# Optimization experiments

Hardware: AMD Instinct MI355X
Metric: run time of the kernel (lower is better)

Reference implementation:

```python
import jax, jax.numpy as jnp
import numpy as np

HIDDEN = 4096
N_HEAD = 16
HEAD_DIM = HIDDEN // N_HEAD          # 256
ROTARY_DIM = HEAD_DIM // 2           # 128 (partial rotary, GPT-J config)
ROPE_BASE = 10000.0
B, S = 4, 1024


def _apply_rope(x, position_ids):
    # x: [B, S, H, D]; rotate first ROTARY_DIM dims, NeoX/rotate-half style.
    rot, pas = x[..., :ROTARY_DIM], x[..., ROTARY_DIM:]
    inv_freq = 1.0 / (ROPE_BASE ** (jnp.arange(0, ROTARY_DIM, 2, dtype=jnp.float32) / ROTARY_DIM))
    ang = position_ids.astype(jnp.float32)[..., None] * inv_freq      # [B, S, R/2]
    cos = jnp.cos(ang)[:, :, None, :]                                  # [B, S, 1, R/2]
    sin = jnp.sin(ang)[:, :, None, :]
    x1, x2 = rot[..., : ROTARY_DIM // 2], rot[..., ROTARY_DIM // 2:]
    rot_out = jnp.concatenate([x1 * cos - x2 * sin, x2 * cos + x1 * sin], axis=-1)
    return jnp.concatenate([rot_out, pas], axis=-1)


def setup_inputs() -> dict:
    key = jax.random.key(0)
    k1, k2, k3 = jax.random.split(key, 3)
    hidden_states = jax.random.normal(k1, (B, S, HIDDEN), dtype=jnp.float32)
    w_qkv = jax.random.normal(k2, (HIDDEN, 3 * HIDDEN), dtype=jnp.float32) * (HIDDEN ** -0.5)
    w_out = jax.random.normal(k3, (HIDDEN, HIDDEN), dtype=jnp.float32) * (HIDDEN ** -0.5)
    position_ids = jnp.broadcast_to(jnp.arange(S, dtype=jnp.int32)[None, :], (B, S))
    return {"position_ids": position_ids, "hidden_states": hidden_states,
            "w_qkv": w_qkv, "w_out": w_out}


def reference(position_ids, hidden_states, w_qkv, w_out):
    qkv = hidden_states @ w_qkv                       # [B, S, 3H]
    q, k, v = jnp.split(qkv, 3, axis=-1)
    q = q.reshape(B, S, N_HEAD, HEAD_DIM)
    k = k.reshape(B, S, N_HEAD, HEAD_DIM)
    v = v.reshape(B, S, N_HEAD, HEAD_DIM)
    q = _apply_rope(q, position_ids)
    k = _apply_rope(k, position_ids)
    scale = HEAD_DIM ** -0.5
    scores = jnp.einsum('bqhd,bkhd->bhqk', q, k) * scale   # [B, H, S, S]
    causal = jnp.tril(jnp.ones((S, S), dtype=bool))
    scores = jnp.where(causal[None, None], scores, jnp.finfo(scores.dtype).min)
    probs = jax.nn.softmax(scores, axis=-1)
    attn = jnp.einsum('bhqk,bkhd->bqhd', probs, v).reshape(B, S, HIDDEN)
    return attn @ w_out
```

## Files before the change

kernel.cpp:

```cpp
#include <hip/hip_runtime.h>
#include <cstdint>

#define HID  4096
#define NHD  16
#define HDIM 256
#define SEQ  1024
#define BB   4
#define N3   12288
#define TOK  4096

typedef unsigned short u16;
typedef __bf16 bf16x8 __attribute__((ext_vector_type(8)));
typedef float  f32x4  __attribute__((ext_vector_type(4)));
typedef float  f32x16 __attribute__((ext_vector_type(16)));

__device__ __forceinline__ u16 f2b(float f) {
    unsigned u = __builtin_bit_cast(unsigned, f);
    u += 0x7fffu + ((u >> 16) & 1u);
    return (u16)(u >> 16);
}
__device__ __forceinline__ float b2f(u16 v) {
    unsigned u = ((unsigned)v) << 16;
    return __builtin_bit_cast(float, u);
}
__device__ __forceinline__ unsigned cvt_pk_bf16(float lo, float hi) {
    unsigned r;
    asm("v_cvt_pk_bf16_f32 %0, %1, %2" : "=v"(r) : "v"(lo), "v"(hi));
    return r;
}

typedef __attribute__((address_space(3))) unsigned       lds_u32;
typedef const __attribute__((address_space(1))) unsigned glb_u32;
__device__ __forceinline__ void async16(const void* g, void* l) {
    __builtin_amdgcn_global_load_lds((glb_u32*)g, (lds_u32*)l, 16, 0, 0);
}

__global__ __launch_bounds__(256) void cast_bf16(const float4* __restrict__ in,
                                                 uint4* __restrict__ out, int n8) {
    int i = blockIdx.x * 256 + threadIdx.x;
    if (i >= n8) return;
    float4 a = in[2 * i], b = in[2 * i + 1];
    union { u16 h[8]; uint4 v; } o;
    o.h[0] = f2b(a.x); o.h[1] = f2b(a.y); o.h[2] = f2b(a.z); o.h[3] = f2b(a.w);
    o.h[4] = f2b(b.x); o.h[5] = f2b(b.y); o.h[6] = f2b(b.z); o.h[7] = f2b(b.w);
    out[i] = o.v;
}

__global__ __launch_bounds__(256) void tcast(const float* __restrict__ in,
                                             u16* __restrict__ out, int R, int C) {
    __shared__ u16 sT[64 * 80];
    const int c0 = blockIdx.x * 64, r0 = blockIdx.y * 64;
    const int t = threadIdx.x;
    const int rr = t >> 4, cc = (t & 15) * 4;
    for (int rnd = 0; rnd < 4; rnd++) {
        int r = rnd * 16 + rr;
        float4 v = *(const float4*)(in + (size_t)(r0 + r) * C + c0 + cc);
        sT[(cc + 0) * 80 + r] = f2b(v.x);
        sT[(cc + 1) * 80 + r] = f2b(v.y);
        sT[(cc + 2) * 80 + r] = f2b(v.z);
        sT[(cc + 3) * 80 + r] = f2b(v.w);
    }
    __syncthreads();
    const int orow = t >> 2, oc = (t & 3) * 16;
    u16* dst = out + (size_t)(c0 + orow) * R + r0 + oc;
    *(uint4*)dst       = *(uint4*)&sT[orow * 80 + oc];
    *(uint4*)(dst + 8) = *(uint4*)&sT[orow * 80 + oc + 8];
}

template <bool OUT_BF16>
__global__ __launch_bounds__(512, 2) void gemm256(const u16* __restrict__ A,
                                                  const u16* __restrict__ Bt,
                                                  void* __restrict__ Cout,
                                                  int M, int N, int K) {
    __shared__ alignas(16) u16 lds[65536];
    const int t = threadIdx.x;
    const int lane = t & 63, w = t >> 6;
    const int wm = w >> 2, wn = w & 3;
    const int fm = lane & 15, g = lane >> 4;

    const int nwg = (int)gridDim.x;
    const int cpx = nwg >> 3;
    const int swz = (((int)blockIdx.x) & 7) * cpx + (((int)blockIdx.x) >> 3);
    const int gm = M >> 8;
    const int mblk = swz % gm, nblk = swz / gm;
    const int m0 = mblk << 8, n0 = nblk << 8;

    const int srow = t >> 2;
    const int schk = ((t & 3) ^ (srow & 3) ^ ((srow >> 2) & 2)) * 8;
    const u16* gA = A  + (size_t)(m0 + srow) * K + schk;
    const u16* gB = Bt + (size_t)(n0 + srow) * K + schk;
    const size_t hstep = (size_t)128 * K;
    const int ldst = t * 8;

    const int cxor = (g ^ (fm & 3) ^ ((fm >> 2) & 2)) * 8;
    const int aoff = (wm * 128 + fm) * 32 + cxor;
    const int boff = 16384 + (wn * 64 + fm) * 32 + cxor;

    f32x4 acc[8][4];
#pragma unroll
    for (int i = 0; i < 8; i++)
#pragma unroll
        for (int j = 0; j < 4; j++) acc[i][j] = f32x4{0.f, 0.f, 0.f, 0.f};

    const int nk = K >> 6;

#define STG_A(BO, KT, KS) do { \
    const u16* s_ = gA + (size_t)(KT) * 64 + (KS) * 32; \
    async16(s_,         &lds[(BO) + (KS) * 8192 + ldst]); \
    async16(s_ + hstep, &lds[(BO) + (KS) * 8192 + 4096 + ldst]); } while (0)
#define STG_B(BO, KT, KS) do { \
    const u16* s_ = gB + (size_t)(KT) * 64 + (KS) * 32; \
    async16(s_,         &lds[(BO) + 16384 + (KS) * 8192 + ldst]); \
    async16(s_ + hstep, &lds[(BO) + 16384 + (KS) * 8192 + 4096 + ldst]); } while (0)

    bf16x8 a0[4], a1[4], bfr[4];

#define LD_A0(BO, KS) { _Pragma("unroll") for (int m_ = 0; m_ < 4; m_++) \
    a0[m_] = *(const bf16x8*)&lds[(BO) + (KS) * 8192 + aoff + m_ * 512]; }
#define LD_A1(BO, KS) { _Pragma("unroll") for (int m_ = 0; m_ < 4; m_++) \
    a1[m_] = *(const bf16x8*)&lds[(BO) + (KS) * 8192 + 2048 + aoff + m_ * 512]; }
#define LD_B(BO, KS) { _Pragma("unroll") for (int n_ = 0; n_ < 4; n_++) \
    bfr[n_] = *(const bf16x8*)&lds[(BO) + (KS) * 8192 + boff + n_ * 512]; }
#define MM(AR, MO) { _Pragma("unroll") for (int m_ = 0; m_ < 4; m_++) \
    _Pragma("unroll") for (int n_ = 0; n_ < 4; n_++) \
    acc[(MO) + m_][n_] = __builtin_amdgcn_mfma_f32_16x16x32_bf16(AR[m_], bfr[n_], acc[(MO) + m_][n_], 0, 0, 0); }
#define BARX __builtin_amdgcn_s_barrier()
#define LGKM0 asm volatile("s_waitcnt lgkmcnt(0)" ::: "memory")
#define VM(N_) asm volatile("s_waitcnt vmcnt(" #N_ ")" ::: "memory")
#define PHASE_MID BARX; LGKM0; __builtin_amdgcn_s_setprio(1)
#define PHASE_END __builtin_amdgcn_s_setprio(0); BARX

    STG_A(0, 0, 0); STG_B(0, 0, 0); STG_A(0, 0, 1); STG_B(0, 0, 1);
    VM(4); BARX;

#pragma unroll 1
    for (int kt = 0; kt < nk - 1; kt++) {
        const int bo = (kt & 1) << 15, nb = bo ^ 32768;
        LD_A0(bo, 0); LD_B(bo, 0);
        STG_A(nb, kt + 1, 0);
        PHASE_MID; MM(a0, 0); PHASE_END;
        LD_A1(bo, 0);
        STG_B(nb, kt + 1, 0);
        VM(4);
        PHASE_MID; MM(a1, 4); PHASE_END;
        LD_A0(bo, 1); LD_B(bo, 1);
        STG_A(nb, kt + 1, 1);
        PHASE_MID; MM(a0, 0); PHASE_END;
        LD_A1(bo, 1);
        STG_B(nb, kt + 1, 1);
        VM(4);
        PHASE_MID; MM(a1, 4); PHASE_END;
    }
    {
        const int bo = ((nk - 1) & 1) << 15;
        LD_A0(bo, 0); LD_B(bo, 0);
        PHASE_MID; MM(a0, 0); PHASE_END;
        LD_A1(bo, 0);
        VM(0);
        PHASE_MID; MM(a1, 4); PHASE_END;
        LD_A0(bo, 1); LD_B(bo, 1);
        PHASE_MID; MM(a0, 0); PHASE_END;
        LD_A1(bo, 1);
        PHASE_MID; MM(a1, 4); PHASE_END;
    }

    const int crow0 = m0 + wm * 128 + g * 4;
    const int ccol = n0 + wn * 64 + fm;
#pragma unroll
    for (int mi = 0; mi < 8; mi++)
#pragma unroll
        for (int r = 0; r < 4; r++) {
            const size_t row = (size_t)(crow0 + mi * 16 + r);
            if (OUT_BF16) {
                u16* p = (u16*)Cout + row * N + ccol;
#pragma unroll
                for (int n_ = 0; n_ < 4; n_++) p[n_ * 16] = f2b(acc[mi][n_][r]);
            } else {
                float* p = (float*)Cout + row * N + ccol;
#pragma unroll
                for (int n_ = 0; n_ < 4; n_++) p[n_ * 16] = acc[mi][n_][r];
            }
        }
#undef STG_A
#undef STG_B
#undef LD_A0
#undef LD_A1
#undef LD_B
#undef MM
#undef BARX
#undef LGKM0
#undef VM
#undef PHASE_MID
#undef PHASE_END
}

__global__ __launch_bounds__(256) void rope_tab(const int* __restrict__ pos_ids,
                                                float2* __restrict__ tab) {
    const int idx = blockIdx.x * 256 + threadIdx.x;
    const int bs = idx >> 6, i = idx & 63;
    const float invf = __expf((float)i * -0.14391156831212787f);
    const float ang = (float)pos_ids[bs] * invf;
    float sn, cs;
    __sincosf(ang, &sn, &cs);
    tab[idx] = make_float2(cs, sn);
}

__global__ __launch_bounds__(256) void rope_relayout(const float2* __restrict__ tab,
                                                     const u16* __restrict__ qkv,
                                                     u16* __restrict__ Qo,
                                                     u16* __restrict__ Ko,
                                                     u16* __restrict__ VTo) {
    __shared__ u16 sV[64 * 256];
    const int st = blockIdx.x, h = blockIdx.y, b = blockIdx.z;
    const int t = threadIdx.x;
    const int sbase = st * 64;

    {
        const u16* vbase = qkv + (size_t)(b * SEQ + sbase) * N3 + 2 * HID + h * HDIM;
        const int dcol = (t & 31) * 8;
        const int tokoff = t >> 5;
#pragma unroll
        for (int r = 0; r < 4; r++)
#pragma unroll
            for (int s8 = 0; s8 < 8; s8++) {
                int tok = r * 16 + s8 * 2 + tokoff;
                async16(vbase + (size_t)tok * N3 + dcol, &sV[r * 4096 + s8 * 512 + t * 8]);
            }
    }

    const int tok = t & 63, part = t >> 6;
    const int s = sbase + tok;
    const int isK = part >> 1, isPass = part & 1;
    const u16* src = qkv + (size_t)(b * SEQ + s) * N3 + isK * HID + h * HDIM + isPass * 128;
    u16* dst = (isK ? Ko : Qo) + ((size_t)((b * NHD + h) * SEQ + s)) * HDIM + isPass * 128;
    if (!isPass) {
        const float2* trow = tab + ((size_t)(b * SEQ + s) << 6);
#pragma unroll
        for (int c = 0; c < 8; c++) {
            bf16x8 xa = *(const bf16x8*)(src + c * 8);
            bf16x8 xb = *(const bf16x8*)(src + 64 + c * 8);
            union { u16 h[8]; uint4 v; } o1, o2;
#pragma unroll
            for (int j = 0; j < 8; j++) {
                float2 t2 = trow[c * 8 + j];
                const float cs = t2.x, sn = t2.y;
                float x1 = (float)xa[j], x2 = (float)xb[j];
                o1.h[j] = f2b(x1 * cs - x2 * sn);
                o2.h[j] = f2b(x2 * cs + x1 * sn);
            }
            *(uint4*)(dst + c * 8)      = o1.v;
            *(uint4*)(dst + 64 + c * 8) = o2.v;
        }
    } else {
        const uint4* s4 = (const uint4*)src;
        uint4* d4 = (uint4*)dst;
#pragma unroll
        for (int c = 0; c < 16; c++) d4[c] = s4[c];
    }

    asm volatile("s_waitcnt vmcnt(0)" ::: "memory");
    __syncthreads();

    u16* vt = VTo + ((size_t)((b * NHD + h) * HDIM + t)) * SEQ + sbase;
#pragma unroll
    for (int g = 0; g < 8; g++) {
        union { u16 h[8]; uint4 v; } o;
#pragma unroll
        for (int j = 0; j < 8; j++) o.h[j] = sV[(g * 8 + j) * 256 + t];
        *(uint4*)(vt + g * 8) = o.v;
    }
}

__global__ __launch_bounds__(256, 2) void attn_fwd(const u16* __restrict__ Q,
                                                   const u16* __restrict__ K,
                                                   const u16* __restrict__ VT,
                                                   u16* __restrict__ attnO) {
    __shared__ u16 sK[2][32 * 256];
    __shared__ u16 sVT[2][32 * 256];
    const int bid = (int)blockIdx.x;
    const int qt8 = (bid < 256) ? (7 - (bid >> 6)) : ((bid - 256) >> 6);
    const int bh = bid & 63, h = bh & 15, b = bh >> 4;
    const int t = threadIdx.x, lane = t & 63, w = t >> 6;
    const int kid = lane & 31, hh = lane >> 5;
    const int qb = qt8 * 128;
    const int qg = qb + w * 32 + kid;
    const int qmaxw = qb + w * 32 + 31;
    const size_t head = ((size_t)(b * NHD + h)) * SEQ * HDIM;
    const u16* kbaseP = K + head;
    const u16* vtbase = VT + head;

    bf16x8 qf[16];
    {
        const u16* qrow = Q + head + (size_t)qg * HDIM + hh * 8;
#pragma unroll
        for (int kk = 0; kk < 16; kk++) qf[kk] = *(const bf16x8*)(qrow + kk * 16);
    }

    f32x16 accO[8];
#pragma unroll
    for (int dg = 0; dg < 8; dg++)
#pragma unroll
        for (int r = 0; r < 16; r++) accO[dg][r] = 0.f;
    float mrow = -1e30f, lrow = 0.f;

    const int nkt = qt8 * 4 + 4;
    const int vsw = (kid >> 3) & 3;

#define STAGE_KV(BUF, KB) do { \
    _Pragma("unroll") for (int r_ = 0; r_ < 4; r_++) { \
        const int key_ = r_ * 8 + (t >> 5); \
        const int ck_  = (t & 31) ^ key_; \
        async16(kbaseP + (size_t)((KB) * 32 + key_) * HDIM + ck_ * 8, \
                &sK[BUF][r_ * 2048 + t * 8]); } \
    _Pragma("unroll") for (int r_ = 0; r_ < 4; r_++) { \
        const int d_ = r_ * 64 + (t >> 2); \
        const int cv_ = (t & 3) ^ ((d_ >> 3) & 3); \
        async16(vtbase + (size_t)d_ * SEQ + (KB) * 32 + cv_ * 8, \
                &sVT[BUF][r_ * 2048 + t * 8]); } } while (0)

    STAGE_KV(0, 0);
    asm volatile("s_waitcnt vmcnt(0)" ::: "memory");
    __syncthreads();

    for (int kb = 0; kb < nkt; kb++) {
        const int cur = kb & 1;
        if (kb + 1 < nkt) STAGE_KV(cur ^ 1, kb + 1);
        if ((kb << 5) <= qmaxw) {
            f32x16 st;
#pragma unroll
            for (int r = 0; r < 16; r++) st[r] = 0.f;
            __builtin_amdgcn_s_setprio(1);
#pragma unroll
            for (int kk = 0; kk < 16; kk++) {
                bf16x8 kf = *(const bf16x8*)&sK[cur][kid * 256 + ((((kk << 1) + hh) ^ kid) << 3)];
                st = __builtin_amdgcn_mfma_f32_32x32x16_bf16(kf, qf[kk], st, 0, 0, 0);
            }
            __builtin_amdgcn_s_setprio(0);
            const int kb32 = kb << 5;
            float p[16];
            float mt = -1e30f;
#pragma unroll
            for (int r = 0; r < 16; r++) {
                const int kgl = kb32 + (r & 3) + 8 * (r >> 2) + 4 * hh;
                p[r] = (kgl <= qg) ? st[r] * 0.0625f : -1e30f;
                mt = fmaxf(mt, p[r]);
            }
            mt = fmaxf(mt, __shfl_xor(mt, 32, 64));
            const float mold = mrow;
            const float mn = fmaxf(mold, mt);
            mrow = mn;
            float rs = 0.f;
#pragma unroll
            for (int r = 0; r < 16; r++) { p[r] = __expf(p[r] - mn); rs += p[r]; }
            rs += __shfl_xor(rs, 32, 64);
            const float alpha = __expf(mold - mn);
            lrow = lrow * alpha + rs;
            if (__any(mn > mold)) {
#pragma unroll
                for (int dg = 0; dg < 8; dg++)
#pragma unroll
                    for (int r = 0; r < 16; r++) accO[dg][r] *= alpha;
            }
            unsigned pw[8];
#pragma unroll
            for (int i = 0; i < 8; i++) pw[i] = cvt_pk_bf16(p[2 * i], p[2 * i + 1]);
            { auto r2 = __builtin_amdgcn_permlane32_swap(pw[0], pw[2], false, false); pw[0] = r2[0]; pw[2] = r2[1]; }
            { auto r2 = __builtin_amdgcn_permlane32_swap(pw[1], pw[3], false, false); pw[1] = r2[0]; pw[3] = r2[1]; }
            { auto r2 = __builtin_amdgcn_permlane32_swap(pw[4], pw[6], false, false); pw[4] = r2[0]; pw[6] = r2[1]; }
            { auto r2 = __builtin_amdgcn_permlane32_swap(pw[5], pw[7], false, false); pw[5] = r2[0]; pw[7] = r2[1]; }
            union { uint4 q; bf16x8 v; } f0, f1;
            f0.q = make_uint4(pw[0], pw[1], pw[2], pw[3]);
            f1.q = make_uint4(pw[4], pw[5], pw[6], pw[7]);
            __builtin_amdgcn_s_setprio(1);
#pragma unroll
            for (int dg = 0; dg < 8; dg++) {
                bf16x8 vf = *(const bf16x8*)&sVT[cur][(dg * 32 + kid) * 32 + ((hh ^ vsw) << 3)];
                accO[dg] = __builtin_amdgcn_mfma_f32_32x32x16_bf16(vf, f0.v, accO[dg], 0, 0, 0);
            }
#pragma unroll
            for (int dg = 0; dg < 8; dg++) {
                bf16x8 vf = *(const bf16x8*)&sVT[cur][(dg * 32 + kid) * 32 + (((2 + hh) ^ vsw) << 3)];
                accO[dg] = __builtin_amdgcn_mfma_f32_32x32x16_bf16(vf, f1.v, accO[dg], 0, 0, 0);
            }
            __builtin_amdgcn_s_setprio(0);
        }
        asm volatile("s_waitcnt vmcnt(0)" ::: "memory");
        __syncthreads();
    }
#undef STAGE_KV
    const float inv = 1.0f / lrow;
    u16* orow = attnO + (size_t)(b * SEQ + qg) * HID + h * HDIM;
#pragma unroll
    for (int dg = 0; dg < 8; dg++)
#pragma unroll
        for (int rq = 0; rq < 4; rq++) {
            union { u16 h4[4]; unsigned long long v; } o;
#pragma unroll
            for (int i = 0; i < 4; i++) o.h4[i] = f2b(accO[dg][rq * 4 + i] * inv);
            *(unsigned long long*)(orow + dg * 32 + rq * 8 + hh * 4) = o.v;
        }
}

extern "C" void kernel_launch(void* const* d_in, const int* in_sizes, int n_in,
                              void* d_out, int out_size, void* d_ws, size_t ws_size,
                              hipStream_t stream) {
    (void)in_sizes; (void)n_in; (void)out_size; (void)ws_size;
    const int*   pos    = (const int*)d_in[0];
    const float* hidden = (const float*)d_in[1];
    const float* wqkv   = (const float*)d_in[2];
    const float* wout   = (const float*)d_in[3];
    float* out = (float*)d_out;
    char* ws = (char*)d_ws;

    u16* hiddenB = (u16*)ws;
    u16* wqkvT   = (u16*)(ws + (size_t)33554432);
    u16* woutT   = (u16*)(ws + (size_t)134217728);
    u16* qkv     = (u16*)(ws + (size_t)167772160);
    u16* Qb    = wqkvT;
    u16* Kb    = wqkvT + 16777216;
    u16* VTb   = wqkvT + 33554432;
    u16* attnB = qkv;
    float2* tabF = (float2*)ws;

    cast_bf16<<<dim3(TOK * HID / 8 / 256), 256, 0, stream>>>(
        (const float4*)hidden, (uint4*)hiddenB, TOK * HID / 8);
    tcast<<<dim3(N3 / 64, HID / 64), 256, 0, stream>>>(wqkv, wqkvT, HID, N3);
    tcast<<<dim3(HID / 64, HID / 64), 256, 0, stream>>>(wout, woutT, HID, HID);
    gemm256<true><<<dim3((TOK / 256) * (N3 / 256)), 512, 0, stream>>>(
        hiddenB, wqkvT, qkv, TOK, N3, HID);
    rope_tab<<<dim3(BB * SEQ * 64 / 256), 256, 0, stream>>>(pos, tabF);
    rope_relayout<<<dim3(SEQ / 64, NHD, BB), 256, 0, stream>>>(tabF, qkv, Qb, Kb, VTb);
    attn_fwd<<<dim3(512), 256, 0, stream>>>(Qb, Kb, VTb, attnB);
    gemm256<false><<<dim3((TOK / 256) * (HID / 256)), 512, 0, stream>>>(
        attnB, woutT, out, TOK, HID, HID);
}
```

Measured before the change: 1.015 ms.

## Restructure GEMM mainloop into 4-stage ring of K=32 LDS slabs

Replaces the double-buffered K=64 tile pipeline (two 32-wide sub-stages per buffer) with a four-slot ring of K=32 slabs, prefetching three slabs ahead. Each slab holds A and B contiguously, and the loop is unrolled by four slabs per outer iteration with a hand-written drain epilogue. The aim is deeper prefetch to better hide global-to-LDS latency behind the MFMA phases. Total LDS use is the same, but the schedule assumes K is a multiple of 128 and has more complex vmcnt accounting.

```diff
diff --git a/kernel.cpp b/kernel.cpp
--- a/kernel.cpp
+++ b/kernel.cpp
@@ -94,7 +94,7 @@
 
     const int cxor = (g ^ (fm & 3) ^ ((fm >> 2) & 2)) * 8;
     const int aoff = (wm * 128 + fm) * 32 + cxor;
-    const int boff = 16384 + (wn * 64 + fm) * 32 + cxor;
+    const int boff = 8192 + (wn * 64 + fm) * 32 + cxor;
 
     f32x4 acc[8][4];
 #pragma unroll
@@ -102,66 +102,73 @@
 #pragma unroll
         for (int j = 0; j < 4; j++) acc[i][j] = f32x4{0.f, 0.f, 0.f, 0.f};
 
-    const int nk = K >> 6;
-
-#define STG_A(BO, KT, KS) do { \
-    const u16* s_ = gA + (size_t)(KT) * 64 + (KS) * 32; \
-    async16(s_,         &lds[(BO) + (KS) * 8192 + ldst]); \
-    async16(s_ + hstep, &lds[(BO) + (KS) * 8192 + 4096 + ldst]); } while (0)
-#define STG_B(BO, KT, KS) do { \
-    const u16* s_ = gB + (size_t)(KT) * 64 + (KS) * 32; \
-    async16(s_,         &lds[(BO) + 16384 + (KS) * 8192 + ldst]); \
-    async16(s_ + hstep, &lds[(BO) + 16384 + (KS) * 8192 + 4096 + ldst]); } while (0)
-
     bf16x8 a0[4], a1[4], bfr[4];
 
-#define LD_A0(BO, KS) { _Pragma("unroll") for (int m_ = 0; m_ < 4; m_++) \
-    a0[m_] = *(const bf16x8*)&lds[(BO) + (KS) * 8192 + aoff + m_ * 512]; }
-#define LD_A1(BO, KS) { _Pragma("unroll") for (int m_ = 0; m_ < 4; m_++) \
-    a1[m_] = *(const bf16x8*)&lds[(BO) + (KS) * 8192 + 2048 + aoff + m_ * 512]; }
-#define LD_B(BO, KS) { _Pragma("unroll") for (int n_ = 0; n_ < 4; n_++) \
-    bfr[n_] = *(const bf16x8*)&lds[(BO) + (KS) * 8192 + boff + n_ * 512]; }
+#define STG_As(S, KE) do { const u16* s_ = gA + (KE); \
+    async16(s_,         &lds[(S) * 16384 + ldst]); \
+    async16(s_ + hstep, &lds[(S) * 16384 + 4096 + ldst]); } while (0)
+#define STG_Bs(S, KE) do { const u16* s_ = gB + (KE); \
+    async16(s_,         &lds[(S) * 16384 + 8192 + ldst]); \
+    async16(s_ + hstep, &lds[(S) * 16384 + 12288 + ldst]); } while (0)
+#define LD_A0s(S) { _Pragma("unroll") for (int m_ = 0; m_ < 4; m_++) \
+    a0[m_] = *(const bf16x8*)&lds[(S) * 16384 + aoff + m_ * 512]; }
+#define LD_A1s(S) { _Pragma("unroll") for (int m_ = 0; m_ < 4; m_++) \
+    a1[m_] = *(const bf16x8*)&lds[(S) * 16384 + 2048 + aoff + m_ * 512]; }
+#define LD_Bs(S)  { _Pragma("unroll") for (int n_ = 0; n_ < 4; n_++) \
+    bfr[n_] = *(const bf16x8*)&lds[(S) * 16384 + boff + n_ * 512]; }
 #define MM(AR, MO) { _Pragma("unroll") for (int m_ = 0; m_ < 4; m_++) \
     _Pragma("unroll") for (int n_ = 0; n_ < 4; n_++) \
     acc[(MO) + m_][n_] = __builtin_amdgcn_mfma_f32_16x16x32_bf16(AR[m_], bfr[n_], acc[(MO) + m_][n_], 0, 0, 0); }
 #define BARX __builtin_amdgcn_s_barrier()
-#define LGKM0 asm volatile("s_waitcnt lgkmcnt(0)" ::: "memory")
 #define VM(N_) asm volatile("s_waitcnt vmcnt(" #N_ ")" ::: "memory")
-#define PHASE_MID BARX; LGKM0; __builtin_amdgcn_s_setprio(1)
+#define PHASE_MID BARX; asm volatile("s_waitcnt lgkmcnt(0)" ::: "memory"); \
+    __builtin_amdgcn_s_setprio(1)
 #define PHASE_END __builtin_amdgcn_s_setprio(0); BARX
 
-    STG_A(0, 0, 0); STG_B(0, 0, 0); STG_A(0, 0, 1); STG_B(0, 0, 1);
-    VM(4); BARX;
-
+    STG_As(0, 0);  STG_Bs(0, 0);
+    STG_As(1, 32); STG_Bs(1, 32);
+    STG_As(2, 64); STG_Bs(2, 64);
+    VM(8); BARX;
+
+    const int nko = (K >> 7) - 1;
 #pragma unroll 1
-    for (int kt = 0; kt < nk - 1; kt++) {
-        const int bo = (kt & 1) << 15, nb = bo ^ 32768;
-        LD_A0(bo, 0); LD_B(bo, 0);
-        STG_A(nb, kt + 1, 0);
+    for (int o = 0; o < nko; o++) {
+        const int kOff = o << 7;
+#pragma unroll
+        for (int j = 0; j < 4; j++) {
+            LD_A0s(j); LD_Bs(j);
+            STG_As((j + 3) & 3, kOff + (j + 3) * 32);
+            PHASE_MID; MM(a0, 0); PHASE_END;
+            LD_A1s(j);
+            STG_Bs((j + 3) & 3, kOff + (j + 3) * 32);
+            VM(8);
+            PHASE_MID; MM(a1, 4); PHASE_END;
+        }
+    }
+    {
+        const int kOff = nko << 7;
+        LD_A0s(0); LD_Bs(0);
+        STG_As(3, kOff + 96);
         PHASE_MID; MM(a0, 0); PHASE_END;
-        LD_A1(bo, 0);
-        STG_B(nb, kt + 1, 0);
+        LD_A1s(0);
+        STG_Bs(3, kOff + 96);
+        VM(8);
+        PHASE_MID; MM(a1, 4); PHASE_END;
+        LD_A0s(1); LD_Bs(1);
+        PHASE_MID; MM(a0, 0); PHASE_END;
+        LD_A1s(1);
         VM(4);
         PHASE_MID; MM(a1, 4); PHASE_END;
-        LD_A0(bo, 1); LD_B(bo, 1);
-        STG_A(nb, kt + 1, 1);
+        LD_A0s(2); LD_Bs(2);
         PHASE_MID; MM(a0, 0); PHASE_END;
-        LD_A1(bo, 1);
-        STG_B(nb, kt + 1, 1);
-        VM(4);
-        PHASE_MID; MM(a1, 4); PHASE_END;
-    }
-    {
-        const int bo = ((nk - 1) & 1) << 15;
-        LD_A0(bo, 0); LD_B(bo, 0);
-        PHASE_MID; MM(a0, 0); PHASE_END;
-        LD_A1(bo, 0);
+        LD_A1s(2);
         VM(0);
         PHASE_MID; MM(a1, 4); PHASE_END;
-        LD_A0(bo, 1); LD_B(bo, 1);
+        LD_A0s(3); LD_Bs(3);
         PHASE_MID; MM(a0, 0); PHASE_END;
-        LD_A1(bo, 1);
-        PHASE_MID; MM(a1, 4); PHASE_END;
+        LD_A1s(3);
+        PHASE_MID; MM(a1, 4);
+        __builtin_amdgcn_s_setprio(0);
     }
 
     const int crow0 = m0 + wm * 128 + g * 4;
@@ -181,14 +188,13 @@
                 for (int n_ = 0; n_ < 4; n_++) p[n_ * 16] = acc[mi][n_][r];
             }
         }
-#undef STG_A
-#undef STG_B
-#undef LD_A0
-#undef LD_A1
-#undef LD_B
+#undef STG_As
+#undef STG_Bs
+#undef LD_A0s
+#undef LD_A1s
+#undef LD_Bs
 #undef MM
 #undef BARX
-#undef LGKM0
 #undef VM
 #undef PHASE_MID
 #undef PHASE_END
```

Measured after the change: 1.004 ms. Within noise of the previous version (-1.0%).
